# Kernel optimization log

Measured on AMD Instinct MI355X. Metric: run time of the kernel, lower is better.

## Reference

```python
import jax, jax.numpy as jnp
import numpy as np

D, S, L, W, H, V = 64, 64, 64, 300, 300, 50000
NEG = jnp.float32(-9999999.0)


def setup_inputs() -> dict:
    key = jax.random.key(0)
    ks = jax.random.split(key, 16)
    n = lambda k, shape, s=0.05: jax.random.normal(k, shape, dtype=jnp.float32) * s
    return {
        "word_indices": jax.random.randint(ks[0], (D, S, L), 0, V),
        "E": n(ks[1], (V, W), 0.1),
        "W_sent": n(ks[2], (H, W)), "b_sent": jnp.zeros((H,), jnp.float32),
        "W_par": n(ks[3], (H, H)), "b_par": jnp.zeros((H,), jnp.float32),
        "W_ch": n(ks[4], (H, H)), "b_ch": jnp.zeros((H,), jnp.float32),
        "w_root": n(ks[5], (H,)), "b_root": jnp.zeros((), jnp.float32),
        "root_embed": n(ks[6], (H,)),
        "W_r": n(ks[7], (H, 3 * H)), "b_r": jnp.zeros((H,), jnp.float32),
        "W_cls": n(ks[8], (2, H)), "b_cls": jnp.zeros((2,), jnp.float32),
    }


def reference(word_indices, E, W_sent, b_sent, W_par, b_par, W_ch, b_ch,
              w_root, b_root, root_embed, W_r, b_r, W_cls, b_cls):
    lrelu = lambda x: jax.nn.leaky_relu(x, 0.01)
    # Ragged pad+gather stage of the original, dense here (all lengths == L)
    word_embed = E[word_indices]                 # [D,S,L,W]
    # 0.5*(X[l-1] + reverse(reverse(X))[l-1]) == X[l-1]; LSTM outputs unused in source
    x_last = word_embed[:, :, -1, :]             # [D,S,W]
    enc = lrelu(x_last @ W_sent.T + b_sent)      # [D,S,H] sentence encodings
    # Pairwise parent-child edge scores (O(S^2) dots in the original loops)
    P = lrelu(enc @ W_par.T + b_par)             # [D,S,H]
    C = lrelu(enc @ W_ch.T + b_ch)               # [D,S,H]
    A = jnp.einsum('dih,djh->dij', P, C)         # [D,S,S]
    A = jnp.where(jnp.eye(S, dtype=bool)[None], NEG, A)
    A = jax.nn.softmax(A, axis=1)                # Softmax(dim=0) per doc: over parents i
    scores = enc @ w_root + b_root               # [D,S] root scores
    fri = jax.nn.softmax(scores, axis=1)         # Softmax(dim=0) over sentences
    # ri[i] = r_embeds([enc_i, sum_k A[k,i]*enc_k + fri_i*root, enc_i*sum_k A[i,k]])
    tmp = jnp.einsum('dki,dkh->dih', A, enc)     # [D,S,H]
    agg = tmp + fri[..., None] * root_embed      # [D,S,H]
    tmp3 = enc * A.sum(axis=2, keepdims=True)    # [D,S,H]
    ri = lrelu(jnp.concatenate([enc, agg, tmp3], axis=-1) @ W_r.T + b_r)  # [D,S,H]
    final = ri.mean(axis=1)                      # [D,H]
    out = final @ W_cls.T + b_cls                # [D,2]
    return out, A, fri
```

## Files before the change

kernel.cpp:

```cpp
#include <hip/hip_runtime.h>
#include <hip/hip_bf16.h>

#define NEG_INF (-9999999.0f)

typedef __attribute__((ext_vector_type(8))) short bf16x8;
typedef __attribute__((ext_vector_type(4))) float f32x4;
typedef unsigned short us;

__device__ __forceinline__ float b2f(us u) {
  union { unsigned int i; float f; } x; x.i = ((unsigned int)u) << 16; return x.f;
}
__device__ __forceinline__ us f2b(float f) {
  union { float f; unsigned int i; } x; x.f = f;
  unsigned int r = x.i + 0x7fffu + ((x.i >> 16) & 1u);
  return (us)(r >> 16);
}
__device__ __forceinline__ float lrelu(float v) { return v > 0.f ? v : 0.01f * v; }
__device__ __forceinline__ bf16x8 ld8(const us* p) { return *reinterpret_cast<const bf16x8*>(p); }

__global__ __launch_bounds__(256) void k_prep(const int* __restrict__ wi, const float* __restrict__ E,
    const float* __restrict__ Ws, const float* __restrict__ Wp, const float* __restrict__ Wc,
    const float* __restrict__ Wr,
    us* __restrict__ Wsb, us* __restrict__ Wpb, us* __restrict__ Wcb, us* __restrict__ Wrb,
    us* __restrict__ xg, us* __restrict__ encb, us* __restrict__ Pb, us* __restrict__ Cb,
    us* __restrict__ encTb) {
  int task = blockIdx.y;
  int gid = blockIdx.x * 256 + threadIdx.x;
  const int stride = 640 * 256;
  if (task < 3) {
    const float* src = (task == 0) ? Ws : (task == 1) ? Wp : Wc;
    us* dst = (task == 0) ? Wsb : (task == 1) ? Wpb : Wcb;
    for (int i = gid; i < 304 * 320; i += stride) {
      int r = i / 320, c = i - r * 320;
      dst[i] = (r < 300 && c < 300) ? f2b(src[r * 300 + c]) : 0;
    }
  } else if (task == 3) {
    for (int i = gid; i < 304 * 928; i += stride) {
      int r = i / 928, c = i - r * 928;
      Wrb[i] = (r < 300 && c < 900) ? f2b(Wr[r * 900 + c]) : 0;
    }
  } else if (task == 4) {
    for (int i = gid; i < 4096 * 320; i += stride) {
      int r = i / 320, c = i - r * 320;
      xg[i] = (c < 300) ? f2b(E[(long)wi[r * 64 + 63] * 300 + c]) : 0;
    }
  } else if (task == 5) {
    for (int i = gid; i < 3 * 4096 * 20; i += stride) {
      int b = i / 81920, rem = i - b * 81920;
      int r = rem / 20, c = 300 + (rem - r * 20);
      us* dst = (b == 0) ? encb : (b == 1) ? Pb : Cb;
      dst[r * 320 + c] = 0;
    }
  } else {
    for (int i = gid; i < 4 * 4096; i += stride)
      encTb[300 * 4096 + i] = 0;
  }
}

template<int NT>
__device__ __forceinline__ void sweep(const us* __restrict__ Ab, int apitch,
    const us* __restrict__ Bb, int bpitch, int m0, int nt0, int lo, int q,
    int ks0, int ksn, f32x4* acc) {
  const us* ar = Ab + (long)(m0 + lo) * apitch + 8 * q + (long)ks0 * 32;
  const us* br[NT];
#pragma unroll
  for (int t = 0; t < NT; ++t)
    br[t] = Bb + (long)((nt0 + t) * 16 + lo) * bpitch + 8 * q + (long)ks0 * 32;
  bf16x8 a0 = ld8(ar), a1 = ld8(ar + 32);
  bf16x8 b0[NT], b1[NT];
#pragma unroll
  for (int t = 0; t < NT; ++t) b0[t] = ld8(br[t]);
#pragma unroll
  for (int t = 0; t < NT; ++t) b1[t] = ld8(br[t] + 32);
  for (int ks = 0; ks < ksn - 2; ++ks) {
    bf16x8 a2 = ld8(ar + (ks + 2) * 32);
    bf16x8 b2[NT];
#pragma unroll
    for (int t = 0; t < NT; ++t) b2[t] = ld8(br[t] + (ks + 2) * 32);
#pragma unroll
    for (int t = 0; t < NT; ++t)
      acc[t] = __builtin_amdgcn_mfma_f32_16x16x32_bf16(a0, b0[t], acc[t], 0, 0, 0);
    a0 = a1; a1 = a2;
#pragma unroll
    for (int t = 0; t < NT; ++t) { b0[t] = b1[t]; b1[t] = b2[t]; }
  }
#pragma unroll
  for (int t = 0; t < NT; ++t)
    acc[t] = __builtin_amdgcn_mfma_f32_16x16x32_bf16(a0, b0[t], acc[t], 0, 0, 0);
#pragma unroll
  for (int t = 0; t < NT; ++t)
    acc[t] = __builtin_amdgcn_mfma_f32_16x16x32_bf16(a1, b1[t], acc[t], 0, 0, 0);
}

template<int NT>
__device__ __forceinline__ void epi_bf16(const f32x4* acc, const float* __restrict__ bias,
    us* __restrict__ outb, us* __restrict__ outT,
    int m0, int nt0, int lo, int q) {
#pragma unroll
  for (int t = 0; t < NT; ++t) {
    int col = (nt0 + t) * 16 + lo;
    if (col >= 300) continue;
    float bb = bias[col];
#pragma unroll
    for (int r = 0; r < 4; ++r) {
      int row = m0 + q * 4 + r;
      us h = f2b(lrelu(acc[t][r] + bb));
      outb[(long)row * 320 + col] = h;
      if (outT) outT[(long)col * 4096 + row] = h;
    }
  }
}

__global__ __launch_bounds__(256) void k_gemm_enc(const us* __restrict__ Ab,
    const us* __restrict__ Bb, const float* __restrict__ bias,
    us* __restrict__ encb, us* __restrict__ encTb) {
  int w = threadIdx.x >> 6, lane = threadIdx.x & 63;
  int lo = lane & 15, q = lane >> 4;
  int m0 = blockIdx.x * 16;
  f32x4 z = {0.f, 0.f, 0.f, 0.f};
  if (w < 3) {
    f32x4 acc[5] = {z, z, z, z, z};
    sweep<5>(Ab, 320, Bb, 320, m0, w * 5, lo, q, 0, 10, acc);
    epi_bf16<5>(acc, bias, encb, encTb, m0, w * 5, lo, q);
  } else {
    f32x4 acc[4] = {z, z, z, z};
    sweep<4>(Ab, 320, Bb, 320, m0, 15, lo, q, 0, 10, acc);
    epi_bf16<4>(acc, bias, encb, encTb, m0, 15, lo, q);
  }
}

__global__ __launch_bounds__(256) void k_gemm_pc(const us* __restrict__ Ab,
    const us* __restrict__ Wpb, const us* __restrict__ Wcb,
    const float* __restrict__ bp, const float* __restrict__ bc,
    us* __restrict__ Pb, us* __restrict__ Cb) {
  int which = blockIdx.y;
  const us* Bb = which ? Wcb : Wpb;
  const float* bias = which ? bc : bp;
  us* outb = which ? Cb : Pb;
  int w = threadIdx.x >> 6, lane = threadIdx.x & 63;
  int lo = lane & 15, q = lane >> 4;
  int m0 = blockIdx.x * 16;
  f32x4 z = {0.f, 0.f, 0.f, 0.f};
  if (w < 3) {
    f32x4 acc[5] = {z, z, z, z, z};
    sweep<5>(Ab, 320, Bb, 320, m0, w * 5, lo, q, 0, 10, acc);
    epi_bf16<5>(acc, bias, outb, (us*)nullptr, m0, w * 5, lo, q);
  } else {
    f32x4 acc[4] = {z, z, z, z};
    sweep<4>(Ab, 320, Bb, 320, m0, 15, lo, q, 0, 10, acc);
    epi_bf16<4>(acc, bias, outb, (us*)nullptr, m0, 15, lo, q);
  }
}

__global__ __launch_bounds__(256) void k_ag(
    const us* __restrict__ Pb, const us* __restrict__ Cb,
    const us* __restrict__ encb, const us* __restrict__ encTb,
    const float* __restrict__ w_root, const float* __restrict__ b_root,
    const float* __restrict__ root,
    float* __restrict__ Aout, float* __restrict__ outF, us* __restrict__ ub) {
  __shared__ float Ls[64][65];
  __shared__ __align__(16) us At[64][72];
  __shared__ float pm[4][64], psum[4][64];
  __shared__ float scores[64], frs[64], rs[64];
  int d = blockIdx.x, t = threadIdx.x;

  {
    int rr = t >> 2, quad = t & 3;
    const us* er = encb + (long)(d * 64 + rr) * 320;
    float s = 0.f;
    for (int h = quad * 4; h + 4 <= 300; h += 16) {
      ushort4 e4 = *reinterpret_cast<const ushort4*>(er + h);
      s = fmaf(b2f(e4.x), w_root[h], s);
      s = fmaf(b2f(e4.y), w_root[h + 1], s);
      s = fmaf(b2f(e4.z), w_root[h + 2], s);
      s = fmaf(b2f(e4.w), w_root[h + 3], s);
    }
    s += __shfl_xor(s, 1);
    s += __shfl_xor(s, 2);
    if (quad == 0) scores[rr] = s + b_root[0];
  }
  __syncthreads();
  if (t < 64) {
    float s = scores[t];
    float m = s;
#pragma unroll
    for (int o = 32; o > 0; o >>= 1) m = fmaxf(m, __shfl_xor(m, o, 64));
    float e = expf(s - m);
    float sum = e;
#pragma unroll
    for (int o = 32; o > 0; o >>= 1) sum += __shfl_xor(sum, o, 64);
    float f = e / sum;
    outF[d * 64 + t] = f;
    frs[t] = f;
  }

  int w = t >> 6, lane = t & 63, lo = lane & 15, q = lane >> 4;
  {
    const us* Pd = Pb + (long)d * 64 * 320;
    const us* Cd = Cb + (long)d * 64 * 320;
    f32x4 z = {0.f, 0.f, 0.f, 0.f};
    f32x4 acc[4] = {z, z, z, z};
    sweep<4>(Pd, 320, Cd, 320, w * 16, 0, lo, q, 0, 10, acc);
#pragma unroll
    for (int t2 = 0; t2 < 4; ++t2) {
#pragma unroll
      for (int r = 0; r < 4; ++r) {
        int i = w * 16 + q * 4 + r, j = t2 * 16 + lo;
        Ls[i][j] = (i == j) ? NEG_INF : acc[t2][r];
      }
    }
  }
  __syncthreads();

  {
    int j = t & 63, p = t >> 6;
    float mx = -3.0e38f;
    for (int i = p * 16; i < p * 16 + 16; ++i) mx = fmaxf(mx, Ls[i][j]);
    pm[p][j] = mx;
    __syncthreads();
    float gmx = fmaxf(fmaxf(pm[0][j], pm[1][j]), fmaxf(pm[2][j], pm[3][j]));
    float s = 0.f;
    for (int i = p * 16; i < p * 16 + 16; ++i) s += expf(Ls[i][j] - gmx);
    psum[p][j] = s;
    __syncthreads();
    float inv = 1.f / (psum[0][j] + psum[1][j] + psum[2][j] + psum[3][j]);
    float* Ad = Aout + (long)d * 4096;
    for (int i = p * 16; i < p * 16 + 16; ++i) {
      float a = expf(Ls[i][j] - gmx) * inv;
      Ad[i * 64 + j] = a;
      At[j][i] = f2b(a);
      Ls[i][j] = a;
    }
  }
  __syncthreads();
  if (t < 64) {
    float s = 0.f;
    for (int j2 = 0; j2 < 64; ++j2) s += Ls[t][j2];
    rs[t] = s;
  }
  __syncthreads();

  {
    bf16x8 av0 = *reinterpret_cast<const bf16x8*>(&At[w * 16 + lo][8 * q]);
    bf16x8 av1 = *reinterpret_cast<const bf16x8*>(&At[w * 16 + lo][32 + 8 * q]);
    const us* brow = encTb + (long)lo * 4096 + d * 64 + 8 * q;
    bf16x8 bv0 = ld8(brow), bv1 = ld8(brow + 32);
    for (int nt = 0; nt < 19; ++nt) {
      bf16x8 nb0, nb1;
      if (nt < 18) {
        const us* nrow = encTb + (long)((nt + 1) * 16 + lo) * 4096 + d * 64 + 8 * q;
        nb0 = ld8(nrow); nb1 = ld8(nrow + 32);
      }
      f32x4 acc = {0.f, 0.f, 0.f, 0.f};
      acc = __builtin_amdgcn_mfma_f32_16x16x32_bf16(av0, bv0, acc, 0, 0, 0);
      acc = __builtin_amdgcn_mfma_f32_16x16x32_bf16(av1, bv1, acc, 0, 0, 0);
      int h = nt * 16 + lo;
      if (h < 300) {
        float rt = root[h];
#pragma unroll
        for (int r = 0; r < 4; ++r) {
          int i = w * 16 + q * 4 + r;
          ub[(long)(d * 64 + i) * 928 + 300 + h] = f2b(acc[r] + frs[i] * rt);
        }
      }
      bv0 = nb0; bv1 = nb1;
    }
  }
  for (int idx = t; idx < 64 * 300; idx += 256) {
    int r = idx / 300, c = idx - r * 300;
    us ev = encb[(long)(d * 64 + r) * 320 + c];
    ub[(long)(d * 64 + r) * 928 + c] = ev;
    ub[(long)(d * 64 + r) * 928 + 600 + c] = f2b(b2f(ev) * rs[r]);
  }
  for (int idx = t; idx < 64 * 28; idx += 256) {
    int r = idx / 28, c = 900 + (idx - r * 28);
    ub[(long)(d * 64 + r) * 928 + c] = 0;
  }
}

__global__ __launch_bounds__(256) void k_gemm_ri(const us* __restrict__ Ab,
    const us* __restrict__ Bb, const float* __restrict__ bias, float* __restrict__ ri) {
  int w = threadIdx.x >> 6, lane = threadIdx.x & 63;
  int lo = lane & 15, q = lane >> 4;
  int m0 = blockIdx.x * 16;
  f32x4 z = {0.f, 0.f, 0.f, 0.f};
  if (w < 3) {
    f32x4 acc[5] = {z, z, z, z, z};
    sweep<5>(Ab, 928, Bb, 928, m0, w * 5, lo, q, 0, 29, acc);
#pragma unroll
    for (int t2 = 0; t2 < 5; ++t2) {
      int col = (w * 5 + t2) * 16 + lo;
      if (col >= 300) continue;
      float bb = bias[col];
#pragma unroll
      for (int r = 0; r < 4; ++r)
        ri[(long)(m0 + q * 4 + r) * 300 + col] = lrelu(acc[t2][r] + bb);
    }
  } else {
    f32x4 acc[4] = {z, z, z, z};
    sweep<4>(Ab, 928, Bb, 928, m0, 15, lo, q, 0, 29, acc);
#pragma unroll
    for (int t2 = 0; t2 < 4; ++t2) {
      int col = (15 + t2) * 16 + lo;
      if (col >= 300) continue;
      float bb = bias[col];
#pragma unroll
      for (int r = 0; r < 4; ++r)
        ri[(long)(m0 + q * 4 + r) * 300 + col] = lrelu(acc[t2][r] + bb);
    }
  }
}

__global__ __launch_bounds__(256) void k_final(const float* __restrict__ ri,
    const float* __restrict__ W_cls, const float* __restrict__ b_cls,
    float* __restrict__ outp) {
  __shared__ float fin[300];
  __shared__ float red[256];
  int d = blockIdx.x, t = threadIdx.x;
  for (int h = t; h < 300; h += 256) {
    float s = 0.f;
    for (int i = 0; i < 64; ++i) s += ri[((d * 64) + i) * 300 + h];
    fin[h] = s * (1.0f / 64.0f);
  }
  __syncthreads();
  for (int c2 = 0; c2 < 2; ++c2) {
    float pth = 0.f;
    for (int h = t; h < 300; h += 256) pth = fmaf(fin[h], W_cls[c2 * 300 + h], pth);
    red[t] = pth;
    __syncthreads();
    for (int o = 128; o > 0; o >>= 1) {
      if (t < o) red[t] += red[t + o];
      __syncthreads();
    }
    if (t == 0) outp[d * 2 + c2] = red[0] + b_cls[c2];
    __syncthreads();
  }
}

extern "C" void kernel_launch(void* const* d_in, const int* in_sizes, int n_in,
                              void* d_out, int out_size, void* d_ws, size_t ws_size,
                              hipStream_t stream) {
  const int*   wi     = (const int*)d_in[0];
  const float* E      = (const float*)d_in[1];
  const float* W_sent = (const float*)d_in[2];
  const float* b_sent = (const float*)d_in[3];
  const float* W_par  = (const float*)d_in[4];
  const float* b_par  = (const float*)d_in[5];
  const float* W_ch   = (const float*)d_in[6];
  const float* b_ch   = (const float*)d_in[7];
  const float* w_root = (const float*)d_in[8];
  const float* b_root = (const float*)d_in[9];
  const float* root_e = (const float*)d_in[10];
  const float* W_r    = (const float*)d_in[11];
  const float* b_r    = (const float*)d_in[12];
  const float* W_cls  = (const float*)d_in[13];
  const float* b_cls  = (const float*)d_in[14];

  us* B = (us*)d_ws;
  us* Wsb   = B;
  us* Wpb   = B + 97280;
  us* Wcb   = B + 194560;
  us* Wrb   = B + 291840;
  us* xg    = B + 573952;
  us* encb  = B + 1884672;
  us* encTb = B + 3195392;
  us* Pb    = B + 4440576;
  us* Cb    = B + 5751296;
  us* ub    = B + 7062016;
  float* ri = (float*)(B + 10863104);

  float* outp = (float*)d_out;
  float* outA = outp + 128;
  float* outF = outp + 128 + 262144;

  k_prep<<<dim3(640, 7), 256, 0, stream>>>(wi, E, W_sent, W_par, W_ch, W_r,
                                           Wsb, Wpb, Wcb, Wrb, xg, encb, Pb, Cb, encTb);
  k_gemm_enc<<<256, 256, 0, stream>>>(xg, Wsb, b_sent, encb, encTb);
  k_gemm_pc<<<dim3(256, 2), 256, 0, stream>>>(encb, Wpb, Wcb, b_par, b_ch, Pb, Cb);
  k_ag<<<64, 256, 0, stream>>>(Pb, Cb, encb, encTb, w_root, b_root, root_e,
                               outA, outF, ub);
  k_gemm_ri<<<256, 256, 0, stream>>>(ub, Wrb, b_r, ri);
  k_final<<<64, 256, 0, stream>>>(ri, W_cls, b_cls, outp);
}
```

Measured before the change: 203.6 us.

## Split attention kernel into column-parallel softmax and separate aggregation kernel

The per-document attention/aggregation kernel, which ran on only 64 blocks, is split into two kernels. k_attn runs a 64x4 grid, with each block handling 16 parent-score columns. It writes A, a transposed bf16 copy of A, and partial row sums to workspace. k_glue2 runs a 64x5 grid that spreads the A^T·enc MFMA tiles and the concat-buffer fill across blocks. The aim is more parallelism on a machine with many CUs, at the cost of an extra launch, redundant root-score computation in each k_attn block, and global round trips for A and the row sums.

```diff
diff --git a/kernel.cpp b/kernel.cpp
--- a/kernel.cpp
+++ b/kernel.cpp
@@ -152,17 +152,16 @@
   }
 }
 
-__global__ __launch_bounds__(256) void k_ag(
-    const us* __restrict__ Pb, const us* __restrict__ Cb,
-    const us* __restrict__ encb, const us* __restrict__ encTb,
+__global__ __launch_bounds__(256) void k_attn(
+    const us* __restrict__ Pb, const us* __restrict__ Cb, const us* __restrict__ encb,
     const float* __restrict__ w_root, const float* __restrict__ b_root,
-    const float* __restrict__ root,
-    float* __restrict__ Aout, float* __restrict__ outF, us* __restrict__ ub) {
-  __shared__ float Ls[64][65];
-  __shared__ __align__(16) us At[64][72];
-  __shared__ float pm[4][64], psum[4][64];
-  __shared__ float scores[64], frs[64], rs[64];
-  int d = blockIdx.x, t = threadIdx.x;
+    float* __restrict__ Aout, float* __restrict__ outF,
+    us* __restrict__ Atb, float* __restrict__ rsp) {
+  __shared__ float Ls[64][17];
+  __shared__ float pm[4][16], psum[4][16];
+  __shared__ float scores[64];
+  int d = blockIdx.x, jg = blockIdx.y, t = threadIdx.x;
+  int w = t >> 6, lane = t & 63, lo = lane & 15, q = lane >> 4;
 
   {
     int rr = t >> 2, quad = t & 3;
@@ -180,7 +179,7 @@
     if (quad == 0) scores[rr] = s + b_root[0];
   }
   __syncthreads();
-  if (t < 64) {
+  if (jg == 0 && t < 64) {
     float s = scores[t];
     float m = s;
 #pragma unroll
@@ -189,92 +188,111 @@
     float sum = e;
 #pragma unroll
     for (int o = 32; o > 0; o >>= 1) sum += __shfl_xor(sum, o, 64);
-    float f = e / sum;
-    outF[d * 64 + t] = f;
-    frs[t] = f;
-  }
-
-  int w = t >> 6, lane = t & 63, lo = lane & 15, q = lane >> 4;
+    outF[d * 64 + t] = e / sum;
+  }
+
   {
     const us* Pd = Pb + (long)d * 64 * 320;
     const us* Cd = Cb + (long)d * 64 * 320;
-    f32x4 z = {0.f, 0.f, 0.f, 0.f};
-    f32x4 acc[4] = {z, z, z, z};
-    sweep<4>(Pd, 320, Cd, 320, w * 16, 0, lo, q, 0, 10, acc);
-#pragma unroll
-    for (int t2 = 0; t2 < 4; ++t2) {
-#pragma unroll
-      for (int r = 0; r < 4; ++r) {
-        int i = w * 16 + q * 4 + r, j = t2 * 16 + lo;
-        Ls[i][j] = (i == j) ? NEG_INF : acc[t2][r];
+    f32x4 acc = {0.f, 0.f, 0.f, 0.f};
+    sweep<1>(Pd, 320, Cd, 320, w * 16, jg, lo, q, 0, 10, &acc);
+#pragma unroll
+    for (int r = 0; r < 4; ++r) {
+      int i = w * 16 + q * 4 + r, j = jg * 16 + lo;
+      Ls[i][lo] = (i == j) ? NEG_INF : acc[r];
+    }
+  }
+  __syncthreads();
+
+  {
+    int col = t & 15, p = t >> 4;
+    if (t < 64) {
+      float mx = -3.0e38f;
+      for (int i = p * 16; i < p * 16 + 16; ++i) mx = fmaxf(mx, Ls[i][col]);
+      pm[p][col] = mx;
+    }
+    __syncthreads();
+    if (t < 64) {
+      float gmx = fmaxf(fmaxf(pm[0][col], pm[1][col]), fmaxf(pm[2][col], pm[3][col]));
+      float s = 0.f;
+      for (int i = p * 16; i < p * 16 + 16; ++i) s += expf(Ls[i][col] - gmx);
+      psum[p][col] = s;
+    }
+    __syncthreads();
+    if (t < 64) {
+      float gmx = fmaxf(fmaxf(pm[0][col], pm[1][col]), fmaxf(pm[2][col], pm[3][col]));
+      float inv = 1.f / (psum[0][col] + psum[1][col] + psum[2][col] + psum[3][col]);
+      int j = jg * 16 + col;
+      float* Ad = Aout + (long)d * 4096;
+      us* Atd = Atb + (long)d * 4096;
+      for (int i = p * 16; i < p * 16 + 16; ++i) {
+        float a = expf(Ls[i][col] - gmx) * inv;
+        Ad[i * 64 + j] = a;
+        Atd[j * 64 + i] = f2b(a);
+        Ls[i][col] = a;
       }
-    }
-  }
-  __syncthreads();
-
-  {
-    int j = t & 63, p = t >> 6;
-    float mx = -3.0e38f;
-    for (int i = p * 16; i < p * 16 + 16; ++i) mx = fmaxf(mx, Ls[i][j]);
-    pm[p][j] = mx;
-    __syncthreads();
-    float gmx = fmaxf(fmaxf(pm[0][j], pm[1][j]), fmaxf(pm[2][j], pm[3][j]));
-    float s = 0.f;
-    for (int i = p * 16; i < p * 16 + 16; ++i) s += expf(Ls[i][j] - gmx);
-    psum[p][j] = s;
-    __syncthreads();
-    float inv = 1.f / (psum[0][j] + psum[1][j] + psum[2][j] + psum[3][j]);
-    float* Ad = Aout + (long)d * 4096;
-    for (int i = p * 16; i < p * 16 + 16; ++i) {
-      float a = expf(Ls[i][j] - gmx) * inv;
-      Ad[i * 64 + j] = a;
-      At[j][i] = f2b(a);
-      Ls[i][j] = a;
     }
   }
   __syncthreads();
   if (t < 64) {
     float s = 0.f;
-    for (int j2 = 0; j2 < 64; ++j2) s += Ls[t][j2];
-    rs[t] = s;
+#pragma unroll
+    for (int c = 0; c < 16; ++c) s += Ls[t][c];
+    rsp[(d * 4 + jg) * 64 + t] = s;
+  }
+}
+
+__global__ __launch_bounds__(256) void k_glue2(
+    const us* __restrict__ Atb, const us* __restrict__ encTb, const us* __restrict__ encb,
+    const float* __restrict__ outF, const float* __restrict__ rsp,
+    const float* __restrict__ root, us* __restrict__ ub) {
+  __shared__ float frs[64], rs[64];
+  int d = blockIdx.x, g = blockIdx.y, t = threadIdx.x;
+  if (t < 64) {
+    frs[t] = outF[d * 64 + t];
+    rs[t] = rsp[(d * 4 + 0) * 64 + t] + rsp[(d * 4 + 1) * 64 + t]
+          + rsp[(d * 4 + 2) * 64 + t] + rsp[(d * 4 + 3) * 64 + t];
   }
   __syncthreads();
-
-  {
-    bf16x8 av0 = *reinterpret_cast<const bf16x8*>(&At[w * 16 + lo][8 * q]);
-    bf16x8 av1 = *reinterpret_cast<const bf16x8*>(&At[w * 16 + lo][32 + 8 * q]);
-    const us* brow = encTb + (long)lo * 4096 + d * 64 + 8 * q;
+  int w = t >> 6, lane = t & 63, lo = lane & 15, q = lane >> 4;
+  int ht = g * 4 + w;
+  if (ht < 19) {
+    const us* Atd = Atb + (long)d * 4096;
+    bf16x8 av0[4], av1[4];
+#pragma unroll
+    for (int mt = 0; mt < 4; ++mt) {
+      av0[mt] = ld8(Atd + (mt * 16 + lo) * 64 + 8 * q);
+      av1[mt] = ld8(Atd + (mt * 16 + lo) * 64 + 32 + 8 * q);
+    }
+    const us* brow = encTb + (long)(ht * 16 + lo) * 4096 + d * 64 + 8 * q;
     bf16x8 bv0 = ld8(brow), bv1 = ld8(brow + 32);
-    for (int nt = 0; nt < 19; ++nt) {
-      bf16x8 nb0, nb1;
-      if (nt < 18) {
-        const us* nrow = encTb + (long)((nt + 1) * 16 + lo) * 4096 + d * 64 + 8 * q;
-        nb0 = ld8(nrow); nb1 = ld8(nrow + 32);
-      }
+    int h = ht * 16 + lo;
+    float rt = (h < 300) ? root[h] : 0.f;
+#pragma unroll
+    for (int mt = 0; mt < 4; ++mt) {
       f32x4 acc = {0.f, 0.f, 0.f, 0.f};
-      acc = __builtin_amdgcn_mfma_f32_16x16x32_bf16(av0, bv0, acc, 0, 0, 0);
-      acc = __builtin_amdgcn_mfma_f32_16x16x32_bf16(av1, bv1, acc, 0, 0, 0);
-      int h = nt * 16 + lo;
+      acc = __builtin_amdgcn_mfma_f32_16x16x32_bf16(av0[mt], bv0, acc, 0, 0, 0);
+      acc = __builtin_amdgcn_mfma_f32_16x16x32_bf16(av1[mt], bv1, acc, 0, 0, 0);
       if (h < 300) {
-        float rt = root[h];
 #pragma unroll
         for (int r = 0; r < 4; ++r) {
-          int i = w * 16 + q * 4 + r;
+          int i = mt * 16 + q * 4 + r;
           ub[(long)(d * 64 + i) * 928 + 300 + h] = f2b(acc[r] + frs[i] * rt);
         }
       }
-      bv0 = nb0; bv1 = nb1;
-    }
-  }
-  for (int idx = t; idx < 64 * 300; idx += 256) {
-    int r = idx / 300, c = idx - r * 300;
+    }
+  }
+  for (int idx = t; idx < 64 * 60; idx += 256) {
+    int r = idx / 60, c = g * 60 + (idx - (idx / 60) * 60);
     us ev = encb[(long)(d * 64 + r) * 320 + c];
     ub[(long)(d * 64 + r) * 928 + c] = ev;
     ub[(long)(d * 64 + r) * 928 + 600 + c] = f2b(b2f(ev) * rs[r]);
   }
-  for (int idx = t; idx < 64 * 28; idx += 256) {
-    int r = idx / 28, c = 900 + (idx - r * 28);
-    ub[(long)(d * 64 + r) * 928 + c] = 0;
+  if (g == 4) {
+    for (int idx = t; idx < 64 * 28; idx += 256) {
+      int r = idx / 28, c = 900 + (idx - r * 28);
+      ub[(long)(d * 64 + r) * 928 + c] = 0;
+    }
   }
 }
 
@@ -367,7 +385,9 @@
   us* Pb    = B + 4440576;
   us* Cb    = B + 5751296;
   us* ub    = B + 7062016;
-  float* ri = (float*)(B + 10863104);
+  us* Atb   = B + 10863104;
+  float* rsp = (float*)(B + 11125248);
+  float* ri  = (float*)(B + 11157760);
 
   float* outp = (float*)d_out;
   float* outA = outp + 128;
@@ -377,8 +397,9 @@
                                            Wsb, Wpb, Wcb, Wrb, xg, encb, Pb, Cb, encTb);
   k_gemm_enc<<<256, 256, 0, stream>>>(xg, Wsb, b_sent, encb, encTb);
   k_gemm_pc<<<dim3(256, 2), 256, 0, stream>>>(encb, Wpb, Wcb, b_par, b_ch, Pb, Cb);
-  k_ag<<<64, 256, 0, stream>>>(Pb, Cb, encb, encTb, w_root, b_root, root_e,
-                               outA, outF, ub);
+  k_attn<<<dim3(64, 4), 256, 0, stream>>>(Pb, Cb, encb, w_root, b_root,
+                                          outA, outF, Atb, rsp);
+  k_glue2<<<dim3(64, 5), 256, 0, stream>>>(Atb, encTb, encb, outF, rsp, root_e, ub);
   k_gemm_ri<<<256, 256, 0, stream>>>(ub, Wrb, b_r, ri);
   k_final<<<64, 256, 0, stream>>>(ri, W_cls, b_cls, outp);
 }
```

Result: faster. 191.6 us (-5.9%).
